# Kernel optimization log

Hardware: AMD Instinct MI355X
Metric: run time of the kernel (lower is better)

Reference implementation:

```python
import jax, jax.numpy as jnp
import numpy as np

N = 50000      # num_nodes
DEG = 16       # avg in-degree
E = N * DEG    # num_edges
IN = 128       # in_feats
HID = 64       # hid_feats
H = 4          # num_heads (conv1)
B = 64         # batch (must equal HID for the original cross_entropy to type-check)
NEG_SLOPE = 0.2


def gat_conv(feat, W, a_l, a_r, b, src, dst, num_nodes):
    """DGL GATConv: per-edge attention + segment softmax over dst + weighted agg."""
    nh, d = a_l.shape
    f = (feat @ W).reshape(num_nodes, nh, d)            # [N,H,D]
    el = jnp.sum(f * a_l[None], axis=-1)                # [N,H]
    er = jnp.sum(f * a_r[None], axis=-1)                # [N,H]
    e = jax.nn.leaky_relu(el[src] + er[dst], negative_slope=NEG_SLOPE)  # [E,H]
    m = jax.ops.segment_max(e, dst, num_segments=num_nodes, indices_are_sorted=True)
    ex = jnp.exp(e - m[dst])
    denom = jax.ops.segment_sum(ex, dst, num_segments=num_nodes, indices_are_sorted=True)
    alpha = ex / denom[dst]                             # [E,H]
    out = jax.ops.segment_sum(alpha[:, :, None] * f[src], dst,
                              num_segments=num_nodes, indices_are_sorted=True)  # [N,H,D]
    return out + b[None]


def setup_inputs() -> dict:
    key = jax.random.key(0)
    ks = jax.random.split(key, 12)
    feat_ids = jax.random.randint(ks[0], (N,), 0, N)
    dst = jnp.repeat(jnp.arange(N), DEG)                # sorted, every node has DEG in-edges
    src = jax.random.randint(ks[1], (E,), 0, N)
    user_ids = jax.random.randint(ks[2], (B,), 0, N)
    item_ids = jax.random.randint(ks[3], (B,), 0, N)
    emb = jax.random.normal(ks[4], (N, IN), jnp.float32)
    W1 = jax.random.normal(ks[5], (IN, H * HID), jnp.float32) * 0.05
    a_l1 = jax.random.normal(ks[6], (H, HID), jnp.float32) * 0.05
    a_r1 = jax.random.normal(ks[7], (H, HID), jnp.float32) * 0.05
    b1 = jnp.zeros((H, HID), jnp.float32)
    W2 = jax.random.normal(ks[8], (H * HID, HID), jnp.float32) * 0.05
    a_l2 = jax.random.normal(ks[9], (1, HID), jnp.float32) * 0.05
    a_r2 = jax.random.normal(ks[10], (1, HID), jnp.float32) * 0.05
    b2 = jnp.zeros((1, HID), jnp.float32)
    return {"feat_ids": feat_ids, "src": src, "dst": dst,
            "user_ids": user_ids, "item_ids": item_ids, "emb": emb,
            "W1": W1, "a_l1": a_l1, "a_r1": a_r1, "b1": b1,
            "W2": W2, "a_l2": a_l2, "a_r2": a_r2, "b2": b2}


def reference(feat_ids, src, dst, user_ids, item_ids, emb,
              W1, a_l1, a_r1, b1, W2, a_l2, a_r2, b2):
    feats = emb[feat_ids]                                 # embedding lookup [N,IN]
    h1 = gat_conv(feats, W1, a_l1, a_r1, b1, src, dst, N).reshape(N, H * HID)
    h1 = jax.nn.relu(h1)
    h2 = gat_conv(h1, W2, a_l2, a_r2, b2, src, dst, N).mean(axis=1)  # [N,HID]
    user_embed = h2[user_ids]                             # [B,HID]
    item_embed = h2[item_ids]
    scores = user_embed * item_embed                      # [B,HID], B == HID
    labels = jnp.eye(B, dtype=scores.dtype)
    loss = jnp.mean(-jnp.sum(labels * jax.nn.log_softmax(scores, axis=-1), axis=-1))
    return (loss, scores, labels)
```

## Files before the change

### kernel.cpp

```cpp
#include <hip/hip_runtime.h>
#include <hip/hip_bf16.h>
#include <math.h>

#define NN   50000
#define DEG  16
#define IN_F 128
#define HID  64
#define NH   4
#define BB   64
#define NT   (NN / 16)

typedef unsigned short u16;
typedef unsigned int   u32;
typedef unsigned char  u8;

typedef __attribute__((ext_vector_type(8))) short  short8;
typedef __attribute__((ext_vector_type(4))) float  f32x4;
typedef __attribute__((ext_vector_type(2))) float  f32x2;

__device__ __forceinline__ u16 f2bf(float x) {
    u32 u = __float_as_uint(x);
    return (u16)((u + 0x7fffu + ((u >> 16) & 1u)) >> 16);
}

__global__ __launch_bounds__(256, 4) void k1_mfma(
    const int* __restrict__ feat_ids, const float* __restrict__ emb,
    const float* __restrict__ W1, const float* __restrict__ a_l1,
    const float* __restrict__ a_r1,
    u8* __restrict__ f1q, float* __restrict__ el1, float* __restrict__ er1)
{
    const int tid  = threadIdx.x;
    const int wave = tid >> 6;
    const int lane = tid & 63;
    const int quad = lane >> 4;
    const int l16  = lane & 15;
    const int colbase = wave * 64;

    short8 bfrag[4][4];
#pragma unroll
    for (int ks = 0; ks < 4; ++ks) {
        const int k0 = ks * 32 + quad * 8;
#pragma unroll
        for (int j = 0; j < 8; ++j) {
            const float4 wv = *(const float4*)(
                W1 + (size_t)(k0 + j) * (NH * HID) + colbase + 4 * l16);
            bfrag[0][ks][j] = (short)f2bf(wv.x);
            bfrag[1][ks][j] = (short)f2bf(wv.y);
            bfrag[2][ks][j] = (short)f2bf(wv.z);
            bfrag[3][ks][j] = (short)f2bf(wv.w);
        }
    }

    const float4 alv = *(const float4*)(a_l1 + colbase + 4 * l16);
    const float4 arv = *(const float4*)(a_r1 + colbase + 4 * l16);

    u8* myf1 = f1q + (size_t)wave * NN * HID;

    __shared__ u16 sA[16][136];

    for (int rt = blockIdx.x; rt < NT; rt += gridDim.x) {
        const int n0 = rt * 16;
        __syncthreads();
        {
            const int r  = tid >> 4;
            const int c8 = (tid & 15) * 8;
            const float* srcp = emb + (size_t)feat_ids[n0 + r] * IN_F + c8;
            const float4 v0 = *(const float4*)(srcp);
            const float4 v1 = *(const float4*)(srcp + 4);
            u32* p = (u32*)&sA[r][c8];
            p[0] = ((u32)f2bf(v0.y) << 16) | f2bf(v0.x);
            p[1] = ((u32)f2bf(v0.w) << 16) | f2bf(v0.z);
            p[2] = ((u32)f2bf(v1.y) << 16) | f2bf(v1.x);
            p[3] = ((u32)f2bf(v1.w) << 16) | f2bf(v1.z);
        }
        __syncthreads();

        f32x4 acc[4];
#pragma unroll
        for (int ct = 0; ct < 4; ++ct) acc[ct] = (f32x4){0.f, 0.f, 0.f, 0.f};

#pragma unroll
        for (int ks = 0; ks < 4; ++ks) {
            const short8 af = *(const short8*)&sA[l16][ks * 32 + quad * 8];
#pragma unroll
            for (int ct = 0; ct < 4; ++ct)
                acc[ct] = __builtin_amdgcn_mfma_f32_16x16x32_bf16(
                    af, bfrag[ct][ks], acc[ct], 0, 0, 0);
        }

        float pl[4], pr[4];
#pragma unroll
        for (int reg = 0; reg < 4; ++reg) {
            const int row = quad * 4 + reg;
            const float v0 = acc[0][reg];
            const float v1 = acc[1][reg];
            const float v2 = acc[2][reg];
            const float v3 = acc[3][reg];
            u32 o = __builtin_amdgcn_cvt_pk_fp8_f32(v0, v1, 0, false);
            o = __builtin_amdgcn_cvt_pk_fp8_f32(v2, v3, o, true);
            *(u32*)(myf1 + (size_t)(n0 + row) * HID + 4 * l16) = o;
            pl[reg] = v0 * alv.x + v1 * alv.y + v2 * alv.z + v3 * alv.w;
            pr[reg] = v0 * arv.x + v1 * arv.y + v2 * arv.z + v3 * arv.w;
        }
#pragma unroll
        for (int o = 8; o > 0; o >>= 1) {
#pragma unroll
            for (int reg = 0; reg < 4; ++reg) {
                pl[reg] += __shfl_down(pl[reg], o);
                pr[reg] += __shfl_down(pr[reg], o);
            }
        }
        if (l16 == 0) {
#pragma unroll
            for (int reg = 0; reg < 4; ++reg) {
                const int n = n0 + quad * 4 + reg;
                el1[(size_t)n * NH + wave] = pl[reg];
                er1[(size_t)n * NH + wave] = pr[reg];
            }
        }
    }
}

__global__ __launch_bounds__(256) void ku_kernel(
    const int* __restrict__ src, const u8* __restrict__ f1q,
    const float* __restrict__ el1, const float* __restrict__ er1,
    const float* __restrict__ b1, const float* __restrict__ W2,
    const float* __restrict__ a_l2, const float* __restrict__ a_r2,
    const float* __restrict__ b2,
    const int* __restrict__ user_ids, const int* __restrict__ item_ids,
    float* __restrict__ h2c)
{
    const int tid  = threadIdx.x;
    const int ns   = tid >> 4;
    const int e    = tid & 15;
    const int wave = tid >> 6;
    const int lane = tid & 63;
    const int quad = lane >> 4;
    const int l16  = lane & 15;
    const int col  = wave * 16 + l16;
    const int u    = blockIdx.x;
    const int id   = (u < BB) ? user_ids[u] : item_ids[u - BB];

    short8 bfrag[8];
#pragma unroll
    for (int ks = 0; ks < 8; ++ks) {
        const int k0 = ks * 32 + quad * 8;
        short8 b;
#pragma unroll
        for (int j = 0; j < 8; ++j)
            b[j] = (short)f2bf(W2[(size_t)(k0 + j) * HID + col]);
        bfrag[ks] = b;
    }
    const float avl = a_l2[col];
    const float avr = a_r2[col];

    __shared__ int   snode[17];
    __shared__ u16   sB[32][264];
    __shared__ float sF[17][68];
    __shared__ float spl[4][16];
    __shared__ float spr1[4];
    __shared__ float sel2[16];
    __shared__ float ser2s;

    if (tid < 17) snode[tid] = (tid < 16) ? src[id * DEG + tid] : id;
    __syncthreads();

#pragma unroll
    for (int pass = 0; pass < 2; ++pass) {
        const int  jrow   = (pass == 0) ? ns : 16;
        const bool active = (pass == 0) || (ns == 0);
        if (active) {
            const int node = snode[jrow];
            const int s    = src[node * DEG + e];
            const float4 elv = *(const float4*)(el1 + (size_t)4 * s);
            const float4 erv = *(const float4*)(er1 + (size_t)4 * node);
            const float elb[4] = {elv.x, elv.y, elv.z, elv.w};
            const float erb[4] = {erv.x, erv.y, erv.z, erv.w};

#pragma unroll
            for (int h = 0; h < NH; ++h) {
                float v = elb[h] + erb[h];
                v = (v > 0.0f) ? v : 0.2f * v;

                float m = v;
                m = fmaxf(m, __shfl_xor(m, 1));
                m = fmaxf(m, __shfl_xor(m, 2));
                m = fmaxf(m, __shfl_xor(m, 4));
                m = fmaxf(m, __shfl_xor(m, 8));
                float ex = expf(v - m);
                float ssum = ex;
                ssum += __shfl_xor(ssum, 1);
                ssum += __shfl_xor(ssum, 2);
                ssum += __shfl_xor(ssum, 4);
                ssum += __shfl_xor(ssum, 8);
                const float alpha = ex / ssum;

                const u8* tab = f1q + (size_t)h * NN * HID;
                float a0 = 0.f, a1 = 0.f, a2 = 0.f, a3 = 0.f;
#pragma unroll
                for (int k = 0; k < DEG; ++k) {
                    const int   sk = __shfl(s, k, 16);
                    const float ak = __shfl(alpha, k, 16);
                    const u32 uu = *(const u32*)(tab + (size_t)sk * HID + 4 * e);
                    const f32x2 lo = __builtin_amdgcn_cvt_pk_f32_fp8(uu, false);
                    const f32x2 hi = __builtin_amdgcn_cvt_pk_f32_fp8(uu, true);
                    a0 += ak * lo.x; a1 += ak * lo.y;
                    a2 += ak * hi.x; a3 += ak * hi.y;
                }
                const float4 bv = *(const float4*)(b1 + h * HID + 4 * e);
                const float r0 = fmaxf(a0 + bv.x, 0.0f);
                const float r1 = fmaxf(a1 + bv.y, 0.0f);
                const float r2 = fmaxf(a2 + bv.z, 0.0f);
                const float r3 = fmaxf(a3 + bv.w, 0.0f);
                u32* dst = (u32*)&sB[jrow][h * 64 + 4 * e];
                dst[0] = ((u32)f2bf(r1) << 16) | f2bf(r0);
                dst[1] = ((u32)f2bf(r3) << 16) | f2bf(r2);
            }
        }
    }
    __syncthreads();

    {
        f32x4 acc = (f32x4){0.f, 0.f, 0.f, 0.f};
#pragma unroll
        for (int ks = 0; ks < 8; ++ks) {
            const short8 af = *(const short8*)&sB[l16][ks * 32 + quad * 8];
            acc = __builtin_amdgcn_mfma_f32_16x16x32_bf16(af, bfrag[ks], acc, 0, 0, 0);
        }
        float pl[4];
#pragma unroll
        for (int reg = 0; reg < 4; ++reg) {
            const int row = quad * 4 + reg;
            const float v = acc[reg];
            sF[row][col] = v;
            pl[reg] = v * avl;
        }
#pragma unroll
        for (int o = 8; o > 0; o >>= 1)
#pragma unroll
            for (int reg = 0; reg < 4; ++reg)
                pl[reg] += __shfl_down(pl[reg], o);
        if (l16 == 0)
#pragma unroll
            for (int reg = 0; reg < 4; ++reg)
                spl[wave][quad * 4 + reg] = pl[reg];
    }
    {
        f32x4 acc = (f32x4){0.f, 0.f, 0.f, 0.f};
#pragma unroll
        for (int ks = 0; ks < 8; ++ks) {
            const short8 af = *(const short8*)&sB[16 + l16][ks * 32 + quad * 8];
            acc = __builtin_amdgcn_mfma_f32_16x16x32_bf16(af, bfrag[ks], acc, 0, 0, 0);
        }
        if (quad == 0) sF[16][col] = acc[0];
        float pr16 = acc[0] * avr;
#pragma unroll
        for (int o = 8; o > 0; o >>= 1) pr16 += __shfl_down(pr16, o);
        if (quad == 0 && l16 == 0) spr1[wave] = pr16;
    }
    __syncthreads();
    if (tid < 16) sel2[tid] = spl[0][tid] + spl[1][tid] + spl[2][tid] + spl[3][tid];
    if (tid == 16) ser2s = spr1[0] + spr1[1] + spr1[2] + spr1[3];
    __syncthreads();

    if (tid < 16) {
        float v = sel2[e] + ser2s;
        v = (v > 0.0f) ? v : 0.2f * v;

        float m = v;
        m = fmaxf(m, __shfl_xor(m, 1));
        m = fmaxf(m, __shfl_xor(m, 2));
        m = fmaxf(m, __shfl_xor(m, 4));
        m = fmaxf(m, __shfl_xor(m, 8));
        float ex = expf(v - m);
        float ssum = ex;
        ssum += __shfl_xor(ssum, 1);
        ssum += __shfl_xor(ssum, 2);
        ssum += __shfl_xor(ssum, 4);
        ssum += __shfl_xor(ssum, 8);
        const float alpha = ex / ssum;

        float a0 = 0.f, a1 = 0.f, a2 = 0.f, a3 = 0.f;
#pragma unroll
        for (int k = 0; k < DEG; ++k) {
            const float ak = __shfl(alpha, k, 16);
            const float* fv = &sF[k][4 * e];
            a0 += ak * fv[0]; a1 += ak * fv[1];
            a2 += ak * fv[2]; a3 += ak * fv[3];
        }
        const float4 bv = *(const float4*)(b2 + 4 * e);
        float4 o = make_float4(a0 + bv.x, a1 + bv.y, a2 + bv.z, a3 + bv.w);
        *(float4*)(h2c + (size_t)u * HID + 4 * e) = o;
    }
}

__global__ __launch_bounds__(256) void kloss(
    const float* __restrict__ h2c,
    float* __restrict__ out_scores, float* __restrict__ out_labels,
    float* __restrict__ out_loss)
{
    const int tid = threadIdx.x;
    const int w = tid >> 6;
    const int j = tid & 63;
    __shared__ float wsum[4];
    float lsum = 0.0f;

#pragma unroll
    for (int r = 0; r < 16; ++r) {
        const int i = r * 4 + w;
        const float sc = h2c[(size_t)i * HID + j] * h2c[(size_t)(BB + i) * HID + j];
        out_scores[i * BB + j] = sc;
        out_labels[i * BB + j] = (i == j) ? 1.0f : 0.0f;

        float mm = sc;
#pragma unroll
        for (int o2 = 32; o2 > 0; o2 >>= 1) mm = fmaxf(mm, __shfl_down(mm, o2));
        mm = __shfl(mm, 0);
        float ee = expf(sc - mm);
#pragma unroll
        for (int o2 = 32; o2 > 0; o2 >>= 1) ee += __shfl_down(ee, o2);
        const float sii = __shfl(sc, i);
        if (j == 0) lsum += -(sii - mm - logf(ee));
    }
    if (j == 0) wsum[w] = lsum;
    __syncthreads();
    if (tid == 0)
        out_loss[0] = (wsum[0] + wsum[1] + wsum[2] + wsum[3]) * (1.0f / (float)BB);
}

extern "C" void kernel_launch(void* const* d_in, const int* in_sizes, int n_in,
                              void* d_out, int out_size, void* d_ws, size_t ws_size,
                              hipStream_t stream)
{
    const int*   feat_ids = (const int*)  d_in[0];
    const int*   src      = (const int*)  d_in[1];
    const int*   user_ids = (const int*)  d_in[3];
    const int*   item_ids = (const int*)  d_in[4];
    const float* emb      = (const float*)d_in[5];
    const float* W1       = (const float*)d_in[6];
    const float* a_l1     = (const float*)d_in[7];
    const float* a_r1     = (const float*)d_in[8];
    const float* b1       = (const float*)d_in[9];
    const float* W2       = (const float*)d_in[10];
    const float* a_l2     = (const float*)d_in[11];
    const float* a_r2     = (const float*)d_in[12];
    const float* b2       = (const float*)d_in[13];

    float* out = (float*)d_out;
    float* out_loss   = out;
    float* out_scores = out + 1;
    float* out_labels = out + 1 + BB * BB;

    u8*    f1q = (u8*)d_ws;
    float* el1 = (float*)(f1q + (size_t)NH * NN * HID);
    float* er1 = el1 + (size_t)NH * NN;
    float* h2c = er1 + (size_t)NH * NN;

    k1_mfma<<<1024, 256, 0, stream>>>(feat_ids, emb, W1, a_l1, a_r1,
                                      f1q, el1, er1);
    ku_kernel<<<2 * BB, 256, 0, stream>>>(src, f1q, el1, er1, b1,
                                          W2, a_l2, a_r2, b2,
                                          user_ids, item_ids, h2c);
    kloss<<<1, 256, 0, stream>>>(h2c, out_scores, out_labels, out_loss);
}
```

Measured before the change: 144.7 us.

## Fuse per-user/item layer-2 and loss kernel into one block per score row

```diff
diff --git a/kernel.cpp b/kernel.cpp
--- a/kernel.cpp
+++ b/kernel.cpp
@@ -27,8 +27,11 @@
     const int* __restrict__ feat_ids, const float* __restrict__ emb,
     const float* __restrict__ W1, const float* __restrict__ a_l1,
     const float* __restrict__ a_r1,
-    u8* __restrict__ f1q, float* __restrict__ el1, float* __restrict__ er1)
+    u8* __restrict__ f1q, float* __restrict__ el1, float* __restrict__ er1,
+    float* __restrict__ out_loss)
 {
+    if (blockIdx.x == 0 && threadIdx.x == 0) out_loss[0] = 0.0f;
+
     const int tid  = threadIdx.x;
     const int wave = tid >> 6;
     const int lane = tid & 63;
@@ -121,14 +124,15 @@
     }
 }
 
-__global__ __launch_bounds__(256) void ku_kernel(
+__global__ __launch_bounds__(256) void kmain(
     const int* __restrict__ src, const u8* __restrict__ f1q,
     const float* __restrict__ el1, const float* __restrict__ er1,
     const float* __restrict__ b1, const float* __restrict__ W2,
     const float* __restrict__ a_l2, const float* __restrict__ a_r2,
     const float* __restrict__ b2,
     const int* __restrict__ user_ids, const int* __restrict__ item_ids,
-    float* __restrict__ h2c)
+    float* __restrict__ out_scores, float* __restrict__ out_labels,
+    float* __restrict__ out_loss)
 {
     const int tid  = threadIdx.x;
     const int ns   = tid >> 4;
@@ -138,8 +142,7 @@
     const int quad = lane >> 4;
     const int l16  = lane & 15;
     const int col  = wave * 16 + l16;
-    const int u    = blockIdx.x;
-    const int id   = (u < BB) ? user_ids[u] : item_ids[u - BB];
+    const int i    = blockIdx.x;
 
     short8 bfrag[8];
 #pragma unroll
@@ -154,68 +157,69 @@
     const float avl = a_l2[col];
     const float avr = a_r2[col];
 
-    __shared__ int   snode[17];
-    __shared__ u16   sB[32][264];
-    __shared__ float sF[17][68];
-    __shared__ float spl[4][16];
-    __shared__ float spr1[4];
-    __shared__ float sel2[16];
-    __shared__ float ser2s;
-
-    if (tid < 17) snode[tid] = (tid < 16) ? src[id * DEG + tid] : id;
-    __syncthreads();
-
-#pragma unroll
-    for (int pass = 0; pass < 2; ++pass) {
-        const int  jrow   = (pass == 0) ? ns : 16;
-        const bool active = (pass == 0) || (ns == 0);
-        if (active) {
-            const int node = snode[jrow];
-            const int s    = src[node * DEG + e];
-            const float4 elv = *(const float4*)(el1 + (size_t)4 * s);
-            const float4 erv = *(const float4*)(er1 + (size_t)4 * node);
-            const float elb[4] = {elv.x, elv.y, elv.z, elv.w};
-            const float erb[4] = {erv.x, erv.y, erv.z, erv.w};
-
-#pragma unroll
-            for (int h = 0; h < NH; ++h) {
-                float v = elb[h] + erb[h];
-                v = (v > 0.0f) ? v : 0.2f * v;
-
-                float m = v;
-                m = fmaxf(m, __shfl_xor(m, 1));
-                m = fmaxf(m, __shfl_xor(m, 2));
-                m = fmaxf(m, __shfl_xor(m, 4));
-                m = fmaxf(m, __shfl_xor(m, 8));
-                float ex = expf(v - m);
-                float ssum = ex;
-                ssum += __shfl_xor(ssum, 1);
-                ssum += __shfl_xor(ssum, 2);
-                ssum += __shfl_xor(ssum, 4);
-                ssum += __shfl_xor(ssum, 8);
-                const float alpha = ex / ssum;
-
-                const u8* tab = f1q + (size_t)h * NN * HID;
-                float a0 = 0.f, a1 = 0.f, a2 = 0.f, a3 = 0.f;
-#pragma unroll
-                for (int k = 0; k < DEG; ++k) {
-                    const int   sk = __shfl(s, k, 16);
-                    const float ak = __shfl(alpha, k, 16);
-                    const u32 uu = *(const u32*)(tab + (size_t)sk * HID + 4 * e);
-                    const f32x2 lo = __builtin_amdgcn_cvt_pk_f32_fp8(uu, false);
-                    const f32x2 hi = __builtin_amdgcn_cvt_pk_f32_fp8(uu, true);
-                    a0 += ak * lo.x; a1 += ak * lo.y;
-                    a2 += ak * hi.x; a3 += ak * hi.y;
-                }
-                const float4 bv = *(const float4*)(b1 + h * HID + 4 * e);
-                const float r0 = fmaxf(a0 + bv.x, 0.0f);
-                const float r1 = fmaxf(a1 + bv.y, 0.0f);
-                const float r2 = fmaxf(a2 + bv.z, 0.0f);
-                const float r3 = fmaxf(a3 + bv.w, 0.0f);
-                u32* dst = (u32*)&sB[jrow][h * 64 + 4 * e];
-                dst[0] = ((u32)f2bf(r1) << 16) | f2bf(r0);
-                dst[1] = ((u32)f2bf(r3) << 16) | f2bf(r2);
+    __shared__ int   snode[34];
+    __shared__ u16   sB[48][264];
+    __shared__ float sF[32][68];
+    __shared__ float spl_u[4][16], spl_i[4][16];
+    __shared__ float spr_u[4], spr_i[4];
+    __shared__ float sel2u[16], sel2i[16];
+    __shared__ float ser2[2];
+    __shared__ float sh2[2][68];
+
+    const int uid = user_ids[i];
+    const int iid = item_ids[i];
+    if (tid < 16)      snode[tid] = src[uid * DEG + tid];
+    else if (tid < 32) snode[tid] = src[iid * DEG + (tid - 16)];
+    else if (tid == 32) snode[32] = uid;
+    else if (tid == 33) snode[33] = iid;
+    __syncthreads();
+
+    for (int jrow = ns; jrow < 34; jrow += 16) {
+        const int node = snode[jrow];
+        const int s    = src[node * DEG + e];
+        const float4 elv = *(const float4*)(el1 + (size_t)4 * s);
+        const float4 erv = *(const float4*)(er1 + (size_t)4 * node);
+        const float elb[4] = {elv.x, elv.y, elv.z, elv.w};
+        const float erb[4] = {erv.x, erv.y, erv.z, erv.w};
+
+#pragma unroll
+        for (int h = 0; h < NH; ++h) {
+            float v = elb[h] + erb[h];
+            v = (v > 0.0f) ? v : 0.2f * v;
+
+            float m = v;
+            m = fmaxf(m, __shfl_xor(m, 1));
+            m = fmaxf(m, __shfl_xor(m, 2));
+            m = fmaxf(m, __shfl_xor(m, 4));
+            m = fmaxf(m, __shfl_xor(m, 8));
+            float ex = expf(v - m);
+            float ssum = ex;
+            ssum += __shfl_xor(ssum, 1);
+            ssum += __shfl_xor(ssum, 2);
+            ssum += __shfl_xor(ssum, 4);
+            ssum += __shfl_xor(ssum, 8);
+            const float alpha = ex / ssum;
+
+            const u8* tab = f1q + (size_t)h * NN * HID;
+            float a0 = 0.f, a1 = 0.f, a2 = 0.f, a3 = 0.f;
+#pragma unroll
+            for (int k = 0; k < DEG; ++k) {
+                const int   sk = __shfl(s, k, 16);
+                const float ak = __shfl(alpha, k, 16);
+                const u32 uu = *(const u32*)(tab + (size_t)sk * HID + 4 * e);
+                const f32x2 lo = __builtin_amdgcn_cvt_pk_f32_fp8(uu, false);
+                const f32x2 hi = __builtin_amdgcn_cvt_pk_f32_fp8(uu, true);
+                a0 += ak * lo.x; a1 += ak * lo.y;
+                a2 += ak * hi.x; a3 += ak * hi.y;
             }
+            const float4 bv = *(const float4*)(b1 + h * HID + 4 * e);
+            const float r0 = fmaxf(a0 + bv.x, 0.0f);
+            const float r1 = fmaxf(a1 + bv.y, 0.0f);
+            const float r2 = fmaxf(a2 + bv.z, 0.0f);
+            const float r3 = fmaxf(a3 + bv.w, 0.0f);
+            u32* dst = (u32*)&sB[jrow][h * 64 + 4 * e];
+            dst[0] = ((u32)f2bf(r1) << 16) | f2bf(r0);
+            dst[1] = ((u32)f2bf(r3) << 16) | f2bf(r2);
         }
     }
     __syncthreads();
@@ -243,7 +247,7 @@
         if (l16 == 0)
 #pragma unroll
             for (int reg = 0; reg < 4; ++reg)
-                spl[wave][quad * 4 + reg] = pl[reg];
+                spl_u[wave][quad * 4 + reg] = pl[reg];
     }
     {
         f32x4 acc = (f32x4){0.f, 0.f, 0.f, 0.f};
@@ -252,19 +256,50 @@
             const short8 af = *(const short8*)&sB[16 + l16][ks * 32 + quad * 8];
             acc = __builtin_amdgcn_mfma_f32_16x16x32_bf16(af, bfrag[ks], acc, 0, 0, 0);
         }
-        if (quad == 0) sF[16][col] = acc[0];
-        float pr16 = acc[0] * avr;
-#pragma unroll
-        for (int o = 8; o > 0; o >>= 1) pr16 += __shfl_down(pr16, o);
-        if (quad == 0 && l16 == 0) spr1[wave] = pr16;
-    }
-    __syncthreads();
-    if (tid < 16) sel2[tid] = spl[0][tid] + spl[1][tid] + spl[2][tid] + spl[3][tid];
-    if (tid == 16) ser2s = spr1[0] + spr1[1] + spr1[2] + spr1[3];
-    __syncthreads();
-
-    if (tid < 16) {
-        float v = sel2[e] + ser2s;
+        float pl[4];
+#pragma unroll
+        for (int reg = 0; reg < 4; ++reg) {
+            const int row = quad * 4 + reg;
+            const float v = acc[reg];
+            sF[16 + row][col] = v;
+            pl[reg] = v * avl;
+        }
+#pragma unroll
+        for (int o = 8; o > 0; o >>= 1)
+#pragma unroll
+            for (int reg = 0; reg < 4; ++reg)
+                pl[reg] += __shfl_down(pl[reg], o);
+        if (l16 == 0)
+#pragma unroll
+            for (int reg = 0; reg < 4; ++reg)
+                spl_i[wave][quad * 4 + reg] = pl[reg];
+    }
+    {
+        f32x4 acc = (f32x4){0.f, 0.f, 0.f, 0.f};
+#pragma unroll
+        for (int ks = 0; ks < 8; ++ks) {
+            const short8 af = *(const short8*)&sB[32 + l16][ks * 32 + quad * 8];
+            acc = __builtin_amdgcn_mfma_f32_16x16x32_bf16(af, bfrag[ks], acc, 0, 0, 0);
+        }
+        float pru = acc[0] * avr;
+        float pri = acc[1] * avr;
+#pragma unroll
+        for (int o = 8; o > 0; o >>= 1) {
+            pru += __shfl_down(pru, o);
+            pri += __shfl_down(pri, o);
+        }
+        if (quad == 0 && l16 == 0) { spr_u[wave] = pru; spr_i[wave] = pri; }
+    }
+    __syncthreads();
+    if (tid < 16)       sel2u[tid] = spl_u[0][tid] + spl_u[1][tid] + spl_u[2][tid] + spl_u[3][tid];
+    else if (tid < 32)  sel2i[tid - 16] = spl_i[0][tid - 16] + spl_i[1][tid - 16] + spl_i[2][tid - 16] + spl_i[3][tid - 16];
+    else if (tid == 32) ser2[0] = spr_u[0] + spr_u[1] + spr_u[2] + spr_u[3];
+    else if (tid == 33) ser2[1] = spr_i[0] + spr_i[1] + spr_i[2] + spr_i[3];
+    __syncthreads();
+
+    if (tid < 32) {
+        const int which = ns;
+        float v = ((which == 0) ? sel2u[e] : sel2i[e]) + ser2[which];
         v = (v > 0.0f) ? v : 0.2f * v;
 
         float m = v;
@@ -284,31 +319,20 @@
 #pragma unroll
         for (int k = 0; k < DEG; ++k) {
             const float ak = __shfl(alpha, k, 16);
-            const float* fv = &sF[k][4 * e];
+            const float* fv = &sF[which * 16 + k][4 * e];
             a0 += ak * fv[0]; a1 += ak * fv[1];
             a2 += ak * fv[2]; a3 += ak * fv[3];
         }
         const float4 bv = *(const float4*)(b2 + 4 * e);
-        float4 o = make_float4(a0 + bv.x, a1 + bv.y, a2 + bv.z, a3 + bv.w);
-        *(float4*)(h2c + (size_t)u * HID + 4 * e) = o;
-    }
-}
-
-__global__ __launch_bounds__(256) void kloss(
-    const float* __restrict__ h2c,
-    float* __restrict__ out_scores, float* __restrict__ out_labels,
-    float* __restrict__ out_loss)
-{
-    const int tid = threadIdx.x;
-    const int w = tid >> 6;
-    const int j = tid & 63;
-    __shared__ float wsum[4];
-    float lsum = 0.0f;
-
-#pragma unroll
-    for (int r = 0; r < 16; ++r) {
-        const int i = r * 4 + w;
-        const float sc = h2c[(size_t)i * HID + j] * h2c[(size_t)(BB + i) * HID + j];
+        float* dst = &sh2[which][4 * e];
+        dst[0] = a0 + bv.x; dst[1] = a1 + bv.y;
+        dst[2] = a2 + bv.z; dst[3] = a3 + bv.w;
+    }
+    __syncthreads();
+
+    if (tid < 64) {
+        const int j = tid;
+        const float sc = sh2[0][j] * sh2[1][j];
         out_scores[i * BB + j] = sc;
         out_labels[i * BB + j] = (i == j) ? 1.0f : 0.0f;
 
@@ -320,12 +344,9 @@
 #pragma unroll
         for (int o2 = 32; o2 > 0; o2 >>= 1) ee += __shfl_down(ee, o2);
         const float sii = __shfl(sc, i);
-        if (j == 0) lsum += -(sii - mm - logf(ee));
-    }
-    if (j == 0) wsum[w] = lsum;
-    __syncthreads();
-    if (tid == 0)
-        out_loss[0] = (wsum[0] + wsum[1] + wsum[2] + wsum[3]) * (1.0f / (float)BB);
+        if (j == 0)
+            atomicAdd(out_loss, -(sii - mm - logf(ee)) * (1.0f / (float)BB));
+    }
 }
 
 extern "C" void kernel_launch(void* const* d_in, const int* in_sizes, int n_in,
@@ -354,12 +375,11 @@
     u8*    f1q = (u8*)d_ws;
     float* el1 = (float*)(f1q + (size_t)NH * NN * HID);
     float* er1 = el1 + (size_t)NH * NN;
-    float* h2c = er1 + (size_t)NH * NN;
 
     k1_mfma<<<1024, 256, 0, stream>>>(feat_ids, emb, W1, a_l1, a_r1,
-                                      f1q, el1, er1);
-    ku_kernel<<<2 * BB, 256, 0, stream>>>(src, f1q, el1, er1, b1,
-                                          W2, a_l2, a_r2, b2,
-                                          user_ids, item_ids, h2c);
-    kloss<<<1, 256, 0, stream>>>(h2c, out_scores, out_labels, out_loss);
+                                      f1q, el1, er1, out_loss);
+    kmain<<<BB, 256, 0, stream>>>(src, f1q, el1, er1, b1,
+                                  W2, a_l2, a_r2, b2,
+                                  user_ids, item_ids,
+                                  out_scores, out_labels, out_loss);
 }
```

Measured after the change: 189.0 us. 1.31x slower.

## Spread ku_kernel head work across a 1024-thread block and batch neighbor gathers

Applied to the files above, without the earlier changes.

```diff
diff --git a/kernel.cpp b/kernel.cpp
--- a/kernel.cpp
+++ b/kernel.cpp
@@ -121,7 +121,7 @@
     }
 }
 
-__global__ __launch_bounds__(256) void ku_kernel(
+__global__ __launch_bounds__(1024, 1) void ku_kernel(
     const int* __restrict__ src, const u8* __restrict__ f1q,
     const float* __restrict__ el1, const float* __restrict__ er1,
     const float* __restrict__ b1, const float* __restrict__ W2,
@@ -130,33 +130,15 @@
     const int* __restrict__ user_ids, const int* __restrict__ item_ids,
     float* __restrict__ h2c)
 {
-    const int tid  = threadIdx.x;
-    const int ns   = tid >> 4;
-    const int e    = tid & 15;
-    const int wave = tid >> 6;
-    const int lane = tid & 63;
-    const int quad = lane >> 4;
-    const int l16  = lane & 15;
-    const int col  = wave * 16 + l16;
-    const int u    = blockIdx.x;
-    const int id   = (u < BB) ? user_ids[u] : item_ids[u - BB];
-
-    short8 bfrag[8];
-#pragma unroll
-    for (int ks = 0; ks < 8; ++ks) {
-        const int k0 = ks * 32 + quad * 8;
-        short8 b;
-#pragma unroll
-        for (int j = 0; j < 8; ++j)
-            b[j] = (short)f2bf(W2[(size_t)(k0 + j) * HID + col]);
-        bfrag[ks] = b;
-    }
-    const float avl = a_l2[col];
-    const float avr = a_r2[col];
+    const int tid = threadIdx.x;
+    const int e   = tid & 15;
+    const int g   = tid >> 4;
+    const int u   = blockIdx.x;
+    const int id  = (u < BB) ? user_ids[u] : item_ids[u - BB];
 
     __shared__ int   snode[17];
     __shared__ u16   sB[32][264];
-    __shared__ float sF[17][68];
+    __shared__ float sF[16][68];
     __shared__ float spl[4][16];
     __shared__ float spr1[4];
     __shared__ float sel2[16];
@@ -167,96 +149,110 @@
 
 #pragma unroll
     for (int pass = 0; pass < 2; ++pass) {
-        const int  jrow   = (pass == 0) ? ns : 16;
-        const bool active = (pass == 0) || (ns == 0);
-        if (active) {
+        const int task = g + pass * 64;
+        if (task < 68) {
+            const int jrow = task >> 2;
+            const int h    = task & 3;
             const int node = snode[jrow];
             const int s    = src[node * DEG + e];
-            const float4 elv = *(const float4*)(el1 + (size_t)4 * s);
-            const float4 erv = *(const float4*)(er1 + (size_t)4 * node);
-            const float elb[4] = {elv.x, elv.y, elv.z, elv.w};
-            const float erb[4] = {erv.x, erv.y, erv.z, erv.w};
-
-#pragma unroll
-            for (int h = 0; h < NH; ++h) {
-                float v = elb[h] + erb[h];
-                v = (v > 0.0f) ? v : 0.2f * v;
-
-                float m = v;
-                m = fmaxf(m, __shfl_xor(m, 1));
-                m = fmaxf(m, __shfl_xor(m, 2));
-                m = fmaxf(m, __shfl_xor(m, 4));
-                m = fmaxf(m, __shfl_xor(m, 8));
-                float ex = expf(v - m);
-                float ssum = ex;
-                ssum += __shfl_xor(ssum, 1);
-                ssum += __shfl_xor(ssum, 2);
-                ssum += __shfl_xor(ssum, 4);
-                ssum += __shfl_xor(ssum, 8);
-                const float alpha = ex / ssum;
-
-                const u8* tab = f1q + (size_t)h * NN * HID;
-                float a0 = 0.f, a1 = 0.f, a2 = 0.f, a3 = 0.f;
-#pragma unroll
-                for (int k = 0; k < DEG; ++k) {
-                    const int   sk = __shfl(s, k, 16);
-                    const float ak = __shfl(alpha, k, 16);
-                    const u32 uu = *(const u32*)(tab + (size_t)sk * HID + 4 * e);
-                    const f32x2 lo = __builtin_amdgcn_cvt_pk_f32_fp8(uu, false);
-                    const f32x2 hi = __builtin_amdgcn_cvt_pk_f32_fp8(uu, true);
-                    a0 += ak * lo.x; a1 += ak * lo.y;
-                    a2 += ak * hi.x; a3 += ak * hi.y;
+            float v = el1[(size_t)4 * s + h] + er1[(size_t)4 * node + h];
+            v = (v > 0.0f) ? v : 0.2f * v;
+
+            float m = v;
+            m = fmaxf(m, __shfl_xor(m, 1));
+            m = fmaxf(m, __shfl_xor(m, 2));
+            m = fmaxf(m, __shfl_xor(m, 4));
+            m = fmaxf(m, __shfl_xor(m, 8));
+            float ex = expf(v - m);
+            float ssum = ex;
+            ssum += __shfl_xor(ssum, 1);
+            ssum += __shfl_xor(ssum, 2);
+            ssum += __shfl_xor(ssum, 4);
+            ssum += __shfl_xor(ssum, 8);
+            const float alpha = ex / ssum;
+
+            int   sk[16];
+            float ak[16];
+#pragma unroll
+            for (int k = 0; k < DEG; ++k) {
+                sk[k] = __shfl(s, k, 16);
+                ak[k] = __shfl(alpha, k, 16);
+            }
+            const u8* tab = f1q + (size_t)h * NN * HID;
+            u32 raw[16];
+#pragma unroll
+            for (int k = 0; k < DEG; ++k)
+                raw[k] = *(const u32*)(tab + (size_t)sk[k] * HID + 4 * e);
+            float a0 = 0.f, a1 = 0.f, a2 = 0.f, a3 = 0.f;
+#pragma unroll
+            for (int k = 0; k < DEG; ++k) {
+                const f32x2 lo = __builtin_amdgcn_cvt_pk_f32_fp8(raw[k], false);
+                const f32x2 hi = __builtin_amdgcn_cvt_pk_f32_fp8(raw[k], true);
+                a0 += ak[k] * lo.x; a1 += ak[k] * lo.y;
+                a2 += ak[k] * hi.x; a3 += ak[k] * hi.y;
+            }
+            const float4 bv = *(const float4*)(b1 + h * HID + 4 * e);
+            const float r0 = fmaxf(a0 + bv.x, 0.0f);
+            const float r1 = fmaxf(a1 + bv.y, 0.0f);
+            const float r2 = fmaxf(a2 + bv.z, 0.0f);
+            const float r3 = fmaxf(a3 + bv.w, 0.0f);
+            u32* dst = (u32*)&sB[jrow][h * 64 + 4 * e];
+            dst[0] = ((u32)f2bf(r1) << 16) | f2bf(r0);
+            dst[1] = ((u32)f2bf(r3) << 16) | f2bf(r2);
+        }
+    }
+    __syncthreads();
+
+    {
+        const int wv   = tid >> 6;
+        const int lane = tid & 63;
+        const int quad = lane >> 4;
+        const int l16  = lane & 15;
+        if (wv < 8) {
+            const int col = (wv & 3) * 16 + l16;
+            short8 bfrag[8];
+#pragma unroll
+            for (int ks = 0; ks < 8; ++ks) {
+                const int k0 = ks * 32 + quad * 8;
+                short8 b;
+#pragma unroll
+                for (int j = 0; j < 8; ++j)
+                    b[j] = (short)f2bf(W2[(size_t)(k0 + j) * HID + col]);
+                bfrag[ks] = b;
+            }
+            const int rbase = (wv < 4) ? 0 : 16;
+            f32x4 acc = (f32x4){0.f, 0.f, 0.f, 0.f};
+#pragma unroll
+            for (int ks = 0; ks < 8; ++ks) {
+                const short8 af = *(const short8*)&sB[rbase + l16][ks * 32 + quad * 8];
+                acc = __builtin_amdgcn_mfma_f32_16x16x32_bf16(af, bfrag[ks], acc, 0, 0, 0);
+            }
+            if (wv < 4) {
+                const float avl = a_l2[col];
+                float pl[4];
+#pragma unroll
+                for (int reg = 0; reg < 4; ++reg) {
+                    const int row = quad * 4 + reg;
+                    sF[row][col] = acc[reg];
+                    pl[reg] = acc[reg] * avl;
                 }
-                const float4 bv = *(const float4*)(b1 + h * HID + 4 * e);
-                const float r0 = fmaxf(a0 + bv.x, 0.0f);
-                const float r1 = fmaxf(a1 + bv.y, 0.0f);
-                const float r2 = fmaxf(a2 + bv.z, 0.0f);
-                const float r3 = fmaxf(a3 + bv.w, 0.0f);
-                u32* dst = (u32*)&sB[jrow][h * 64 + 4 * e];
-                dst[0] = ((u32)f2bf(r1) << 16) | f2bf(r0);
-                dst[1] = ((u32)f2bf(r3) << 16) | f2bf(r2);
-            }
-        }
-    }
-    __syncthreads();
-
-    {
-        f32x4 acc = (f32x4){0.f, 0.f, 0.f, 0.f};
-#pragma unroll
-        for (int ks = 0; ks < 8; ++ks) {
-            const short8 af = *(const short8*)&sB[l16][ks * 32 + quad * 8];
-            acc = __builtin_amdgcn_mfma_f32_16x16x32_bf16(af, bfrag[ks], acc, 0, 0, 0);
-        }
-        float pl[4];
-#pragma unroll
-        for (int reg = 0; reg < 4; ++reg) {
-            const int row = quad * 4 + reg;
-            const float v = acc[reg];
-            sF[row][col] = v;
-            pl[reg] = v * avl;
-        }
-#pragma unroll
-        for (int o = 8; o > 0; o >>= 1)
-#pragma unroll
-            for (int reg = 0; reg < 4; ++reg)
-                pl[reg] += __shfl_down(pl[reg], o);
-        if (l16 == 0)
-#pragma unroll
-            for (int reg = 0; reg < 4; ++reg)
-                spl[wave][quad * 4 + reg] = pl[reg];
-    }
-    {
-        f32x4 acc = (f32x4){0.f, 0.f, 0.f, 0.f};
-#pragma unroll
-        for (int ks = 0; ks < 8; ++ks) {
-            const short8 af = *(const short8*)&sB[16 + l16][ks * 32 + quad * 8];
-            acc = __builtin_amdgcn_mfma_f32_16x16x32_bf16(af, bfrag[ks], acc, 0, 0, 0);
-        }
-        if (quad == 0) sF[16][col] = acc[0];
-        float pr16 = acc[0] * avr;
-#pragma unroll
-        for (int o = 8; o > 0; o >>= 1) pr16 += __shfl_down(pr16, o);
-        if (quad == 0 && l16 == 0) spr1[wave] = pr16;
+#pragma unroll
+                for (int o = 8; o > 0; o >>= 1)
+#pragma unroll
+                    for (int reg = 0; reg < 4; ++reg)
+                        pl[reg] += __shfl_down(pl[reg], o);
+                if (l16 == 0)
+#pragma unroll
+                    for (int reg = 0; reg < 4; ++reg)
+                        spl[wv][quad * 4 + reg] = pl[reg];
+            } else {
+                const float avr = a_r2[col];
+                float pr16 = acc[0] * avr;
+#pragma unroll
+                for (int o = 8; o > 0; o >>= 1) pr16 += __shfl_down(pr16, o);
+                if (quad == 0 && l16 == 0) spr1[wv - 4] = pr16;
+            }
+        }
     }
     __syncthreads();
     if (tid < 16) sel2[tid] = spl[0][tid] + spl[1][tid] + spl[2][tid] + spl[3][tid];
@@ -358,8 +354,8 @@
 
     k1_mfma<<<1024, 256, 0, stream>>>(feat_ids, emb, W1, a_l1, a_r1,
                                       f1q, el1, er1);
-    ku_kernel<<<2 * BB, 256, 0, stream>>>(src, f1q, el1, er1, b1,
-                                          W2, a_l2, a_r2, b2,
-                                          user_ids, item_ids, h2c);
+    ku_kernel<<<2 * BB, 1024, 0, stream>>>(src, f1q, el1, er1, b1,
+                                           W2, a_l2, a_r2, b2,
+                                           user_ids, item_ids, h2c);
     kloss<<<1, 256, 0, stream>>>(h2c, out_scores, out_labels, out_loss);
 }
```

New measurement: 136.7 us. -5.5%, faster.
